# Kernel tuning notes

Measured on AMD Instinct MI355X. Metric: run time of the kernel, lower is better.

## Reference

```python
import jax, jax.numpy as jnp
import numpy as np

B, T, H, NUM_TAGS = 16, 2048, 1024, 74
RATE_HEAD, RATE_MID = 0.88, 0.7


def _make_segments(rng):
    """Build ragged word segmentation as dense index/mask tensors.

    word_idx[b, t]  : index j of the word covering char position t
    is_head[b, t]   : True iff t is the first char of its word segment
    valid_mask[b, t]: True iff t < length of utterance b
    """
    word_idx = np.zeros((B, T), dtype=np.int32)
    is_head = np.zeros((B, T), dtype=bool)
    valid = np.zeros((B, T), dtype=bool)
    for b in range(B):
        length = int(rng.integers(T // 2, T + 1))
        s, j = 0, 0
        while s < length:
            seg = int(rng.integers(1, 5))  # jieba-like segments of 1..4 chars
            seg = min(seg, length - s)
            word_idx[b, s:s + seg] = j
            is_head[b, s] = True
            valid[b, s:s + seg] = True
            s += seg
            j += 1
    return word_idx, is_head, valid


def setup_inputs() -> dict:
    key = jax.random.key(0)
    k1, k2, k3 = jax.random.split(key, 3)
    rng = np.random.default_rng(0)
    word_idx, is_head, valid = _make_segments(rng)
    return {
        "out_char": jax.random.normal(k1, (B, T, H), dtype=jnp.float32),
        "out_word": jax.random.normal(k2, (B, T, H), dtype=jnp.float32),
        "word_idx": jnp.asarray(word_idx),
        "is_head": jnp.asarray(is_head),
        "valid_mask": jnp.asarray(valid),
        "W_out": jax.random.normal(k3, (H, NUM_TAGS), dtype=jnp.float32) / np.sqrt(H),
        "b_out": jnp.zeros((NUM_TAGS,), dtype=jnp.float32),
    }


def reference(out_char, out_word, word_idx, is_head, valid_mask, W_out, b_out):
    # Feat_Merge: fused gather-scale-scatter over ragged word segments.
    # rate = rate_head on the first char of each segment, rate_mid elsewhere.
    rate = jnp.where(is_head, RATE_HEAD, RATE_MID).astype(out_char.dtype)  # [B, T]
    gathered = jnp.take_along_axis(out_word, word_idx[:, :, None], axis=1)  # [B, T, H]
    feat = gathered * rate[:, :, None] + out_char * (1.0 - rate)[:, :, None]
    feat = jnp.where(valid_mask[:, :, None], feat, 0.0)  # zeros beyond length (as in feat_B init)
    # Output tagging projection (dropout p=0 at inference)
    logits = jnp.einsum("bth,hk->btk", feat, W_out) + b_out  # [B, T, num_tags]
    return logits
```

## Files before the change

kernel.cpp:

```cpp
#include <hip/hip_runtime.h>
#include <hip/hip_bf16.h>

#define TT 2048
#define HH 1024
#define NTAGS 74
#define NPAD 80
#define CHK 64
#define NCH (HH / CHK)
#define MROWS 128
#define THREADS 512

typedef __bf16 bf16x8 __attribute__((ext_vector_type(8)));
typedef float f32x4 __attribute__((ext_vector_type(4)));

__global__ __launch_bounds__(256) void prep_w_kernel(const float* __restrict__ W,
                                                     __bf16* __restrict__ Wt) {
    __shared__ float tile[64][80];
    const int k0 = blockIdx.x * 64;
    const int tid = threadIdx.x;
    for (int i = tid; i < 64 * NTAGS; i += 256) {
        int k = i / NTAGS, n = i - k * NTAGS;
        tile[k][n] = W[(k0 + k) * NTAGS + n];
    }
    __syncthreads();
    for (int i = tid; i < NPAD * 64; i += 256) {
        int n = i >> 6, kk = i & 63;
        float v = (n < NTAGS) ? tile[kk][n] : 0.0f;
        Wt[n * HH + k0 + kk] = (__bf16)v;
    }
}

__global__ __launch_bounds__(512, 1) void slu_main(const float* __restrict__ out_char,
                                                   const float* __restrict__ out_word,
                                                   const int* __restrict__ word_idx,
                                                   const int* __restrict__ is_head,
                                                   const int* __restrict__ valid_mask,
                                                   const __bf16* __restrict__ Wt,
                                                   const float* __restrict__ b_out,
                                                   float* __restrict__ out) {
    __shared__ __align__(16) char smem[53248];
    const int tid = threadIdx.x;
    const int wv = tid >> 6;
    const int lane = tid & 63;
    const int l15 = lane & 15;
    const int kgrp = lane >> 4;

    const int bid = blockIdx.x;
    const int batch = bid >> 4;
    const int j = bid & 15;
    const int fb = batch * TT + j * 64;
    const int bb = batch * TT + TT - (j + 1) * 64;

    const int rloc = tid >> 2;
    const int q = tid & 3;
    const int r = (rloc < 64) ? (fb + rloc) : (bb + (rloc - 64));
    const int widx = word_idx[r];
    const int val = valid_mask[r];
    const float rt = is_head[r] ? 0.88f : 0.70f;
    const float rate = val ? rt : 0.0f;
    const float crate = val ? (1.0f - rt) : 0.0f;
    const float* cptr = out_char + (size_t)r * HH + q * 16;
    const float* wptr = out_word + ((size_t)batch * TT + widx) * HH + q * 16;
    const int asw = (rloc & 7) << 4;
    const int awr0 = (rloc * 128 + q * 32) ^ asw;
    const int awr1 = (rloc * 128 + q * 32 + 16) ^ asw;

    const int wn0 = tid >> 3, wsb = tid & 7;
    const __bf16* wgp0 = Wt + (size_t)wn0 * HH + wsb * 8;
    const __bf16* wgp1 = wgp0 + 64 * HH;
    const int wsw = (wn0 & 7) << 4;
    const int wwr0 = (wn0 * 128 + wsb * 16) ^ wsw;
    const int wwr1 = ((wn0 + 64) * 128 + wsb * 16) ^ wsw;
    const bool w2 = (tid < 128);

    const int fsw = (l15 & 7) << 4;
    const int arow = wv * 16 + l15;
    int aoff[2], woff[2][5];
#pragma unroll
    for (int s = 0; s < 2; ++s) {
        aoff[s] = (arow * 128 + s * 64 + kgrp * 16) ^ fsw;
#pragma unroll
        for (int nt = 0; nt < 5; ++nt)
            woff[s][nt] = ((nt * 16 + l15) * 128 + s * 64 + kgrp * 16) ^ fsw;
    }

    f32x4 acc[5];
#pragma unroll
    for (int nt = 0; nt < 5; ++nt) acc[nt] = (f32x4){0.f, 0.f, 0.f, 0.f};

    float4 ac[4], aw[4];
    bf16x8 wreg0, wreg1;

    {
        float4 c0[4], w0[4];
        if (val) {
#pragma unroll
            for (int i = 0; i < 4; ++i) {
                c0[i] = *(const float4*)(cptr + i * 4);
                w0[i] = *(const float4*)(wptr + i * 4);
            }
        }
        bf16x8 wr0 = *(const bf16x8*)(wgp0);
        bf16x8 wr1 = w2 ? *(const bf16x8*)(wgp1) : (bf16x8)0;
        bf16x8 f0, f1;
        if (val) {
#pragma unroll
            for (int i = 0; i < 2; ++i) {
                f0[i * 4 + 0] = (__bf16)(w0[i].x * rate + c0[i].x * crate);
                f0[i * 4 + 1] = (__bf16)(w0[i].y * rate + c0[i].y * crate);
                f0[i * 4 + 2] = (__bf16)(w0[i].z * rate + c0[i].z * crate);
                f0[i * 4 + 3] = (__bf16)(w0[i].w * rate + c0[i].w * crate);
                f1[i * 4 + 0] = (__bf16)(w0[i + 2].x * rate + c0[i + 2].x * crate);
                f1[i * 4 + 1] = (__bf16)(w0[i + 2].y * rate + c0[i + 2].y * crate);
                f1[i * 4 + 2] = (__bf16)(w0[i + 2].z * rate + c0[i + 2].z * crate);
                f1[i * 4 + 3] = (__bf16)(w0[i + 2].w * rate + c0[i + 2].w * crate);
            }
        } else {
            f0 = (bf16x8)0; f1 = (bf16x8)0;
        }
        *(bf16x8*)(smem + awr0) = f0;
        *(bf16x8*)(smem + awr1) = f1;
        *(bf16x8*)(smem + 32768 + wwr0) = wr0;
        if (w2) *(bf16x8*)(smem + 32768 + wwr1) = wr1;
        if (val) {
#pragma unroll
            for (int i = 0; i < 4; ++i) {
                ac[i] = *(const float4*)(cptr + CHK + i * 4);
                aw[i] = *(const float4*)(wptr + CHK + i * 4);
            }
        }
        wreg0 = *(const bf16x8*)(wgp0 + CHK);
        wreg1 = w2 ? *(const bf16x8*)(wgp1 + CHK) : (bf16x8)0;
    }
    __syncthreads();

    for (int ch = 0; ch < NCH; ++ch) {
        if (ch + 1 < NCH) {
            char* An = smem + ((ch + 1) & 1) * 16384;
            char* Wn = smem + 32768 + ((ch + 1) & 1) * 10240;
            bf16x8 f0, f1;
            if (val) {
#pragma unroll
                for (int i = 0; i < 2; ++i) {
                    f0[i * 4 + 0] = (__bf16)(aw[i].x * rate + ac[i].x * crate);
                    f0[i * 4 + 1] = (__bf16)(aw[i].y * rate + ac[i].y * crate);
                    f0[i * 4 + 2] = (__bf16)(aw[i].z * rate + ac[i].z * crate);
                    f0[i * 4 + 3] = (__bf16)(aw[i].w * rate + ac[i].w * crate);
                    f1[i * 4 + 0] = (__bf16)(aw[i + 2].x * rate + ac[i + 2].x * crate);
                    f1[i * 4 + 1] = (__bf16)(aw[i + 2].y * rate + ac[i + 2].y * crate);
                    f1[i * 4 + 2] = (__bf16)(aw[i + 2].z * rate + ac[i + 2].z * crate);
                    f1[i * 4 + 3] = (__bf16)(aw[i + 2].w * rate + ac[i + 2].w * crate);
                }
            } else {
                f0 = (bf16x8)0; f1 = (bf16x8)0;
            }
            *(bf16x8*)(An + awr0) = f0;
            *(bf16x8*)(An + awr1) = f1;
            *(bf16x8*)(Wn + wwr0) = wreg0;
            if (w2) *(bf16x8*)(Wn + wwr1) = wreg1;
        }
        if (ch + 2 < NCH) {
            const int ko = (ch + 2) * CHK;
            if (val) {
#pragma unroll
                for (int i = 0; i < 4; ++i) {
                    ac[i] = *(const float4*)(cptr + ko + i * 4);
                    aw[i] = *(const float4*)(wptr + ko + i * 4);
                }
            }
            wreg0 = *(const bf16x8*)(wgp0 + ko);
            wreg1 = w2 ? *(const bf16x8*)(wgp1 + ko) : (bf16x8)0;
        }
        const char* Ab = smem + (ch & 1) * 16384;
        const char* Wb = smem + 32768 + (ch & 1) * 10240;
#pragma unroll
        for (int s = 0; s < 2; ++s) {
            bf16x8 a = *(const bf16x8*)(Ab + aoff[s]);
#pragma unroll
            for (int nt = 0; nt < 5; ++nt) {
                bf16x8 bw = *(const bf16x8*)(Wb + woff[s][nt]);
                acc[nt] = __builtin_amdgcn_mfma_f32_16x16x32_bf16(a, bw, acc[nt], 0, 0, 0);
            }
        }
        __syncthreads();
    }

    const int obase = (wv < 4) ? (fb + wv * 16) : (bb + (wv - 4) * 16);
    const int orow = obase + kgrp * 4;
#pragma unroll
    for (int nt = 0; nt < 5; ++nt) {
        const int col = nt * 16 + l15;
        if (col < NTAGS) {
            const float bias = b_out[col];
#pragma unroll
            for (int i = 0; i < 4; ++i) {
                out[(size_t)(orow + i) * NTAGS + col] = acc[nt][i] + bias;
            }
        }
    }
}

extern "C" void kernel_launch(void* const* d_in, const int* in_sizes, int n_in,
                              void* d_out, int out_size, void* d_ws, size_t ws_size,
                              hipStream_t stream) {
    const float* out_char = (const float*)d_in[0];
    const float* out_word = (const float*)d_in[1];
    const int* word_idx = (const int*)d_in[2];
    const int* is_head = (const int*)d_in[3];
    const int* valid_mask = (const int*)d_in[4];
    const float* W_out = (const float*)d_in[5];
    const float* b_out = (const float*)d_in[6];
    float* out = (float*)d_out;
    __bf16* Wt = (__bf16*)d_ws;

    prep_w_kernel<<<HH / 64, 256, 0, stream>>>(W_out, Wt);

    const int rows = 16 * TT;
    slu_main<<<rows / MROWS, THREADS, 0, stream>>>(out_char, out_word, word_idx, is_head,
                                                   valid_mask, Wt, b_out, out);
}
```

Before: 40.62 us.

## Retile main kernel to 256 threads, 2 blocks/CU, XCD mapping, skip invalid tiles

Halves the block to 256 threads with two blocks per CU and halves the K chunk to 32. Each wave now computes 32 rows, so one W fragment load is shared across two MFMAs. The A tile is triple-buffered and W double-buffered in smaller shared memory. Blocks get contiguous 128-row tiles remapped so neighbouring tiles spread across the 8 XCDs, replacing the earlier front/back pairing used for load balance. Tiles where every row is invalid exit early after writing only the bias, which skips loads and MFMA work in exchange for possible imbalance between blocks.

```diff
diff --git a/kernel.cpp b/kernel.cpp
--- a/kernel.cpp
+++ b/kernel.cpp
@@ -5,10 +5,11 @@
 #define HH 1024
 #define NTAGS 74
 #define NPAD 80
-#define CHK 64
+#define CHK 32
 #define NCH (HH / CHK)
 #define MROWS 128
-#define THREADS 512
+#define THREADS 256
+#define NXCD 8
 
 typedef __bf16 bf16x8 __attribute__((ext_vector_type(8)));
 typedef float f32x4 __attribute__((ext_vector_type(4)));
@@ -30,7 +31,7 @@
     }
 }
 
-__global__ __launch_bounds__(512, 1) void slu_main(const float* __restrict__ out_char,
+__global__ __launch_bounds__(256, 2) void slu_main(const float* __restrict__ out_char,
                                                    const float* __restrict__ out_word,
                                                    const int* __restrict__ word_idx,
                                                    const int* __restrict__ is_head,
@@ -38,7 +39,7 @@
                                                    const __bf16* __restrict__ Wt,
                                                    const float* __restrict__ b_out,
                                                    float* __restrict__ out) {
-    __shared__ __align__(16) char smem[53248];
+    __shared__ __align__(16) char smem[34816];
     const int tid = threadIdx.x;
     const int wv = tid >> 6;
     const int lane = tid & 63;
@@ -46,47 +47,55 @@
     const int kgrp = lane >> 4;
 
     const int bid = blockIdx.x;
-    const int batch = bid >> 4;
-    const int j = bid & 15;
-    const int fb = batch * TT + j * 64;
-    const int bb = batch * TT + TT - (j + 1) * 64;
-
-    const int rloc = tid >> 2;
-    const int q = tid & 3;
-    const int r = (rloc < 64) ? (fb + rloc) : (bb + (rloc - 64));
+    const int rb = (bid & (NXCD - 1)) * (256 / NXCD) + (bid >> 3);
+    const int rowbase = rb * MROWS;
+    const int batch = rowbase >> 11;
+    const size_t batbase = (size_t)batch * TT;
+
+    const int myv = (tid < MROWS) ? valid_mask[rowbase + tid] : 0;
+    if (!__syncthreads_or(myv)) {
+        for (int i = tid; i < MROWS * NTAGS; i += THREADS) {
+            const int rr = i / NTAGS, cc = i - rr * NTAGS;
+            out[(size_t)(rowbase + rr) * NTAGS + cc] = b_out[cc];
+        }
+        return;
+    }
+
+    const int srow = tid >> 1;
+    const int qh = tid & 1;
+    const int r = rowbase + srow;
     const int widx = word_idx[r];
     const int val = valid_mask[r];
     const float rt = is_head[r] ? 0.88f : 0.70f;
     const float rate = val ? rt : 0.0f;
     const float crate = val ? (1.0f - rt) : 0.0f;
-    const float* cptr = out_char + (size_t)r * HH + q * 16;
-    const float* wptr = out_word + ((size_t)batch * TT + widx) * HH + q * 16;
-    const int asw = (rloc & 7) << 4;
-    const int awr0 = (rloc * 128 + q * 32) ^ asw;
-    const int awr1 = (rloc * 128 + q * 32 + 16) ^ asw;
-
-    const int wn0 = tid >> 3, wsb = tid & 7;
-    const __bf16* wgp0 = Wt + (size_t)wn0 * HH + wsb * 8;
+    const float* cptr = out_char + (size_t)r * HH + qh * 16;
+    const float* wptr = out_word + (batbase + widx) * HH + qh * 16;
+    const int akey = (srow & 7) << 4;
+    const int awr0 = (srow * 64 + qh * 32) ^ akey;
+    const int awr1 = (srow * 64 + qh * 32 + 16) ^ akey;
+
+    const int wn0 = tid >> 2, wsu = tid & 3;
+    const __bf16* wgp0 = Wt + (size_t)wn0 * HH + wsu * 8;
     const __bf16* wgp1 = wgp0 + 64 * HH;
-    const int wsw = (wn0 & 7) << 4;
-    const int wwr0 = (wn0 * 128 + wsb * 16) ^ wsw;
-    const int wwr1 = ((wn0 + 64) * 128 + wsb * 16) ^ wsw;
-    const bool w2 = (tid < 128);
-
-    const int fsw = (l15 & 7) << 4;
-    const int arow = wv * 16 + l15;
-    int aoff[2], woff[2][5];
-#pragma unroll
-    for (int s = 0; s < 2; ++s) {
-        aoff[s] = (arow * 128 + s * 64 + kgrp * 16) ^ fsw;
-#pragma unroll
-        for (int nt = 0; nt < 5; ++nt)
-            woff[s][nt] = ((nt * 16 + l15) * 128 + s * 64 + kgrp * 16) ^ fsw;
-    }
-
-    f32x4 acc[5];
-#pragma unroll
-    for (int nt = 0; nt < 5; ++nt) acc[nt] = (f32x4){0.f, 0.f, 0.f, 0.f};
+    const int wwr0 = (wn0 * 64 + wsu * 16) ^ ((wn0 & 7) << 4);
+    const int wwr1 = ((wn0 + 64) * 64 + wsu * 16) ^ ((wn0 & 7) << 4);
+    const bool w2 = (tid < 64);
+
+    const int fkey = (l15 & 7) << 4;
+    int aoff[2], woff[5];
+#pragma unroll
+    for (int s = 0; s < 2; ++s)
+        aoff[s] = ((wv * 32 + s * 16 + l15) * 64 + kgrp * 16) ^ fkey;
+#pragma unroll
+    for (int nt = 0; nt < 5; ++nt)
+        woff[nt] = ((nt * 16 + l15) * 64 + kgrp * 16) ^ fkey;
+
+    f32x4 acc[2][5];
+#pragma unroll
+    for (int s = 0; s < 2; ++s)
+#pragma unroll
+        for (int nt = 0; nt < 5; ++nt) acc[s][nt] = (f32x4){0.f, 0.f, 0.f, 0.f};
 
     float4 ac[4], aw[4];
     bf16x8 wreg0, wreg1;
@@ -120,8 +129,8 @@
         }
         *(bf16x8*)(smem + awr0) = f0;
         *(bf16x8*)(smem + awr1) = f1;
-        *(bf16x8*)(smem + 32768 + wwr0) = wr0;
-        if (w2) *(bf16x8*)(smem + 32768 + wwr1) = wr1;
+        *(bf16x8*)(smem + 24576 + wwr0) = wr0;
+        if (w2) *(bf16x8*)(smem + 24576 + wwr1) = wr1;
         if (val) {
 #pragma unroll
             for (int i = 0; i < 4; ++i) {
@@ -136,8 +145,8 @@
 
     for (int ch = 0; ch < NCH; ++ch) {
         if (ch + 1 < NCH) {
-            char* An = smem + ((ch + 1) & 1) * 16384;
-            char* Wn = smem + 32768 + ((ch + 1) & 1) * 10240;
+            char* An = smem + ((ch + 1) % 3) * 8192;
+            char* Wn = smem + 24576 + ((ch + 1) & 1) * 5120;
             bf16x8 f0, f1;
             if (val) {
 #pragma unroll
@@ -171,30 +180,31 @@
             wreg0 = *(const bf16x8*)(wgp0 + ko);
             wreg1 = w2 ? *(const bf16x8*)(wgp1 + ko) : (bf16x8)0;
         }
-        const char* Ab = smem + (ch & 1) * 16384;
-        const char* Wb = smem + 32768 + (ch & 1) * 10240;
-#pragma unroll
-        for (int s = 0; s < 2; ++s) {
-            bf16x8 a = *(const bf16x8*)(Ab + aoff[s]);
-#pragma unroll
-            for (int nt = 0; nt < 5; ++nt) {
-                bf16x8 bw = *(const bf16x8*)(Wb + woff[s][nt]);
-                acc[nt] = __builtin_amdgcn_mfma_f32_16x16x32_bf16(a, bw, acc[nt], 0, 0, 0);
-            }
+        const char* Ab = smem + (ch % 3) * 8192;
+        const char* Wb = smem + 24576 + (ch & 1) * 5120;
+        bf16x8 a0 = *(const bf16x8*)(Ab + aoff[0]);
+        bf16x8 a1 = *(const bf16x8*)(Ab + aoff[1]);
+#pragma unroll
+        for (int nt = 0; nt < 5; ++nt) {
+            bf16x8 bw = *(const bf16x8*)(Wb + woff[nt]);
+            acc[0][nt] = __builtin_amdgcn_mfma_f32_16x16x32_bf16(a0, bw, acc[0][nt], 0, 0, 0);
+            acc[1][nt] = __builtin_amdgcn_mfma_f32_16x16x32_bf16(a1, bw, acc[1][nt], 0, 0, 0);
         }
         __syncthreads();
     }
 
-    const int obase = (wv < 4) ? (fb + wv * 16) : (bb + (wv - 4) * 16);
-    const int orow = obase + kgrp * 4;
-#pragma unroll
-    for (int nt = 0; nt < 5; ++nt) {
-        const int col = nt * 16 + l15;
-        if (col < NTAGS) {
-            const float bias = b_out[col];
-#pragma unroll
-            for (int i = 0; i < 4; ++i) {
-                out[(size_t)(orow + i) * NTAGS + col] = acc[nt][i] + bias;
+#pragma unroll
+    for (int s = 0; s < 2; ++s) {
+        const int orow = rowbase + wv * 32 + s * 16 + kgrp * 4;
+#pragma unroll
+        for (int nt = 0; nt < 5; ++nt) {
+            const int col = nt * 16 + l15;
+            if (col < NTAGS) {
+                const float bias = b_out[col];
+#pragma unroll
+                for (int i = 0; i < 4; ++i) {
+                    out[(size_t)(orow + i) * NTAGS + col] = acc[s][nt][i] + bias;
+                }
             }
         }
     }
```

After: 47.18 us. +16.2%, slower.
